# Optimization experiments

Hardware: AMD Instinct MI355X
Metric: run time of the kernel (lower is better)

Reference implementation:

```python
import jax, jax.numpy as jnp
import numpy as np

N, E = 50000, 800000
IN, C, H, EDIM = 128, 16, 8, 8  # in_channels, out_channels per head, heads, edge_dim
NEG_SLOPE = 0.2


def setup_inputs() -> dict:
    key = jax.random.key(0)
    ks = jax.random.split(key, 10)
    g = 1.0 / np.sqrt(IN)
    inp = {
        "x": jax.random.normal(ks[0], (N, IN), dtype=jnp.float32),
        "edge_index": jax.random.randint(ks[1], (2, E), 0, N, dtype=jnp.int64),
        "edge_attr": jax.random.normal(ks[2], (E, EDIM), dtype=jnp.float32),
        # GATv2Conv params (share_weights=False): lin_l, lin_r with bias, lin_edge no bias
        "W_l": jax.random.normal(ks[3], (IN, H * C), dtype=jnp.float32) * g,
        "b_l": jnp.zeros((H * C,), dtype=jnp.float32),
        "W_r": jax.random.normal(ks[4], (IN, H * C), dtype=jnp.float32) * g,
        "b_r": jnp.zeros((H * C,), dtype=jnp.float32),
        "W_e": jax.random.normal(ks[5], (EDIM, H * C), dtype=jnp.float32) * (1.0 / np.sqrt(EDIM)),
        "att": jax.random.normal(ks[6], (H, C), dtype=jnp.float32) * (1.0 / np.sqrt(C)),
        "bias": jnp.zeros((H * C,), dtype=jnp.float32),
    }
    return inp


def _gatv2_forward(x, edge_index, edge_attr, W_l, b_l, W_r, b_r, W_e, att, bias):
    n = x.shape[0]
    x_l = (x @ W_l + b_l).reshape(n, H, C)  # source transform
    x_r = (x @ W_r + b_r).reshape(n, H, C)  # target transform

    # add self-loops; edge_attr fill_value='mean' (PyG GATv2Conv default)
    loop = jnp.arange(n, dtype=edge_index.dtype)
    src = jnp.concatenate([edge_index[0], loop])
    dst = jnp.concatenate([edge_index[1], loop])
    loop_attr = jnp.broadcast_to(edge_attr.mean(axis=0, keepdims=True), (n, EDIM))
    e_attr = jnp.concatenate([edge_attr, loop_attr], axis=0)  # [E+N, EDIM]

    e_emb = (e_attr @ W_e).reshape(-1, H, C)  # [E+N, H, C]
    m = x_l[src] + x_r[dst] + e_emb          # gather per edge
    m = jax.nn.leaky_relu(m, NEG_SLOPE)
    logit = jnp.einsum("ehc,hc->eh", m, att)  # [E+N, H]

    # destination-grouped (scatter) softmax
    seg_max = jax.ops.segment_max(logit, dst, num_segments=n)
    expd = jnp.exp(logit - seg_max[dst])
    seg_sum = jax.ops.segment_sum(expd, dst, num_segments=n)
    alpha = expd / (seg_sum[dst] + 1e-16)     # [E+N, H]

    msg = alpha[:, :, None] * x_l[src]        # [E+N, H, C]
    out = jax.ops.segment_sum(msg, dst, num_segments=n)  # [N, H, C]
    return out.reshape(n, H * C) + bias       # concat heads + bias


def reference(x, edge_index, edge_attr, W_l, b_l, W_r, b_r, W_e, att, bias):
    return _gatv2_forward(x, edge_index, edge_attr, W_l, b_l, W_r, b_r, W_e, att, bias)
```

## Files before the change

kernel.cpp:

```cpp
#include <hip/hip_runtime.h>

#define NHEAD 8
#define CH    16
#define HC    128
#define INC   128
#define EDIM  8
#define NEG   0.2f

typedef _Float16 h8 __attribute__((ext_vector_type(8)));
typedef _Float16 h4 __attribute__((ext_vector_type(4)));
typedef _Float16 h2 __attribute__((ext_vector_type(2)));
typedef float    f4 __attribute__((ext_vector_type(4)));

__device__ __forceinline__ float lrelu(float v) { return v > 0.f ? v : NEG * v; }

__device__ __forceinline__ float dot2(h2 a, h2 b, float c) {
#if __has_builtin(__builtin_amdgcn_fdot2)
    return __builtin_amdgcn_fdot2(a, b, c, false);
#else
    return c + (float)a[0] * (float)b[0] + (float)a[1] * (float)b[1];
#endif
}

__global__ void k_packW(const float* __restrict__ Wl, const float* __restrict__ Wr,
                        _Float16* __restrict__ packed) {
    int id = blockIdx.x * blockDim.x + threadIdx.x;
    int l  = id & 63;
    int kb = (id >> 6) & 3;
    int t  = id >> 8;
    int col = t * 16 + (l & 15);
    const float* W = (col < HC) ? Wl : Wr;
    int c = col & 127;
    int kbase = kb * 32 + (l >> 4) * 8;
    _Float16* dst = packed + (size_t)id * 8;
    #pragma unroll
    for (int j = 0; j < 8; ++j) dst[j] = (_Float16)W[(size_t)(kbase + j) * HC + c];
}

__global__ __launch_bounds__(256) void k_phase1(
        const float* __restrict__ x, const _Float16* __restrict__ packed,
        const float* __restrict__ bl, const float* __restrict__ br,
        _Float16* __restrict__ xh,
        const int* __restrict__ ei, const float* __restrict__ ea,
        int* __restrict__ cnt, int* __restrict__ rank, float* __restrict__ attr_sum,
        int N, int E, int gemmBlocks) {
    __shared__ _Float16 st[16][264];
    __shared__ float red[4][8];

    if ((int)blockIdx.x < gemmBlocks) {
        int nb0 = blockIdx.x * 128;
        int w  = threadIdx.x >> 6;
        int l  = threadIdx.x & 63;

        const h8* pk = (const h8*)packed;
        h8 bfrag[4][4];
        #pragma unroll
        for (int t4 = 0; t4 < 4; ++t4)
            #pragma unroll
            for (int kb = 0; kb < 4; ++kb)
                bfrag[t4][kb] = pk[(size_t)(((w * 4 + t4) * 4 + kb) * 64 + l)];

        float bv[4];
        int cl = l & 15;
        #pragma unroll
        for (int t4 = 0; t4 < 4; ++t4) {
            int col = w * 64 + t4 * 16 + cl;
            bv[t4] = (col < HC) ? bl[col] : br[col - HC];
        }

        int g = l >> 4;
        int r0 = g * 4;
        for (int mt = 0; mt < 8; ++mt) {
            int m0 = nb0 + mt * 16;
            if (m0 >= N) break;
            int row = m0 + cl; if (row >= N) row = N - 1;
            const float* xp = x + (size_t)row * INC + g * 8;
            h8 afrag[4];
            #pragma unroll
            for (int kb = 0; kb < 4; ++kb) {
                float4 u = *(const float4*)(xp + kb * 32);
                float4 v = *(const float4*)(xp + kb * 32 + 4);
                h8 a;
                a[0] = (_Float16)u.x; a[1] = (_Float16)u.y; a[2] = (_Float16)u.z; a[3] = (_Float16)u.w;
                a[4] = (_Float16)v.x; a[5] = (_Float16)v.y; a[6] = (_Float16)v.z; a[7] = (_Float16)v.w;
                afrag[kb] = a;
            }
            f4 acc[4];
            #pragma unroll
            for (int t4 = 0; t4 < 4; ++t4) { f4 z = {0.f, 0.f, 0.f, 0.f}; acc[t4] = z; }
            #pragma unroll
            for (int kb = 0; kb < 4; ++kb)
                #pragma unroll
                for (int t4 = 0; t4 < 4; ++t4)
                    acc[t4] = __builtin_amdgcn_mfma_f32_16x16x32_f16(afrag[kb], bfrag[t4][kb], acc[t4], 0, 0, 0);
            #pragma unroll
            for (int t4 = 0; t4 < 4; ++t4) {
                int col = w * 64 + t4 * 16 + cl;
                #pragma unroll
                for (int j = 0; j < 4; ++j)
                    st[r0 + j][col] = (_Float16)(acc[t4][j] + bv[t4]);
            }
            __syncthreads();
            #pragma unroll
            for (int q = 0; q < 2; ++q) {
                int cch = threadIdx.x + 256 * q;
                int r = cch >> 5, ch = (cch & 31) * 8;
                int node = m0 + r;
                if (node < N) *(h8*)(xh + (size_t)node * 256 + ch) = *(const h8*)&st[r][ch];
            }
            __syncthreads();
        }
    } else {
        int t = (blockIdx.x - gemmBlocks) * 256 + threadIdx.x;
        float av[8] = {0.f, 0.f, 0.f, 0.f, 0.f, 0.f, 0.f, 0.f};
        if (t < E) {
            rank[t] = atomicAdd(&cnt[ei[E + t]], 1);
            float4 a0 = *(const float4*)(ea + (size_t)t * EDIM);
            float4 a1 = *(const float4*)(ea + (size_t)t * EDIM + 4);
            av[0] = a0.x; av[1] = a0.y; av[2] = a0.z; av[3] = a0.w;
            av[4] = a1.x; av[5] = a1.y; av[6] = a1.z; av[7] = a1.w;
        }
        #pragma unroll
        for (int m = 1; m < 64; m <<= 1) {
            #pragma unroll
            for (int k = 0; k < 8; ++k) av[k] += __shfl_xor(av[k], m);
        }
        int lane = threadIdx.x & 63, wid = threadIdx.x >> 6;
        if (lane == 0) {
            #pragma unroll
            for (int k = 0; k < 8; ++k) red[wid][k] = av[k];
        }
        __syncthreads();
        if (threadIdx.x < 8) {
            float s = red[0][threadIdx.x] + red[1][threadIdx.x] + red[2][threadIdx.x] + red[3][threadIdx.x];
            atomicAdd(&attr_sum[threadIdx.x], s);
        }
    }
}

__global__ void k_scan1(const int* __restrict__ cnt, int* __restrict__ off,
                        int* __restrict__ bsum, int N) {
    __shared__ int wpre[16];
    int i = blockIdx.x * 1024 + threadIdx.x;
    int lane = threadIdx.x & 63, wid = threadIdx.x >> 6;
    int v = (i < N) ? cnt[i] : 0;
    int s = v;
    #pragma unroll
    for (int d = 1; d < 64; d <<= 1) {
        int t = __shfl_up(s, d);
        if (lane >= d) s += t;
    }
    if (lane == 63) wpre[wid] = s;
    __syncthreads();
    if (threadIdx.x == 0) {
        int run = 0;
        #pragma unroll
        for (int q = 0; q < 16; ++q) { int t = wpre[q]; wpre[q] = run; run += t; }
        bsum[blockIdx.x] = run;
    }
    __syncthreads();
    if (i <= N) off[i] = wpre[wid] + s - v;
}

__global__ void k_scan2lo(const int* __restrict__ bsum, int* __restrict__ bsx, int nb,
                          const float* __restrict__ attr_sum, const float* __restrict__ We,
                          const float* __restrict__ att, float* __restrict__ loop_emb,
                          _Float16* __restrict__ We16, _Float16* __restrict__ att16,
                          float invE) {
    int tid = threadIdx.x;
    if (tid < 64) {
        int v = (tid < nb) ? bsum[tid] : 0;
        int s = v;
        #pragma unroll
        for (int d = 1; d < 64; d <<= 1) {
            int t = __shfl_up(s, d);
            if (tid >= d) s += t;
        }
        if (tid < nb) bsx[tid] = s - v;
    } else if (tid < 192) {
        int j = tid - 64;
        float acc = 0.f;
        #pragma unroll
        for (int d = 0; d < EDIM; ++d) {
            float w = We[d * HC + j];
            acc += attr_sum[d] * invE * w;
            We16[d * HC + j] = (_Float16)w;
        }
        loop_emb[j] = acc;
        att16[j] = (_Float16)att[j];
    }
}

__global__ void k_scatter(const int* __restrict__ ei, const float* __restrict__ ea,
                          const int* __restrict__ off, const int* __restrict__ bsx,
                          const int* __restrict__ rank,
                          int* __restrict__ esrc, h8* __restrict__ eac, int E) {
    int t = blockIdx.x * blockDim.x + threadIdx.x;
    if (t >= E) return;
    int dst = ei[E + t];
    int pos = off[dst] + bsx[dst >> 10] + rank[t];
    esrc[pos] = ei[t];
    float4 a0 = *(const float4*)(ea + (size_t)t * EDIM);
    float4 a1 = *(const float4*)(ea + (size_t)t * EDIM + 4);
    h8 v;
    v[0] = (_Float16)a0.x; v[1] = (_Float16)a0.y; v[2] = (_Float16)a0.z; v[3] = (_Float16)a0.w;
    v[4] = (_Float16)a1.x; v[5] = (_Float16)a1.y; v[6] = (_Float16)a1.z; v[7] = (_Float16)a1.w;
    eac[pos] = v;
}

__global__ __launch_bounds__(256) void k_gather(
        const int* __restrict__ esrc, const h8* __restrict__ eac,
        const _Float16* __restrict__ We16, const _Float16* __restrict__ att16,
        const float* __restrict__ attf, const _Float16* __restrict__ xh,
        const float* __restrict__ loop_emb, const float* __restrict__ bias,
        const int* __restrict__ off, const int* __restrict__ bsx,
        float* __restrict__ out, int N) {
    int wave = (blockIdx.x * blockDim.x + threadIdx.x) >> 6;
    int lane = threadIdx.x & 63;
    if (wave >= N) return;
    int dst = __builtin_amdgcn_readfirstlane(wave);
    int qid = lane >> 4;
    int l   = lane & 15;
    int c0  = l * 8;

    h8 we8[EDIM];
    #pragma unroll
    for (int d = 0; d < EDIM; ++d) we8[d] = *(const h8*)(We16 + d * HC + c0);
    h2 att2[4];
    #pragma unroll
    for (int k = 0; k < 4; ++k) att2[k] = *(const h2*)(att16 + c0 + 2 * k);
    h8 xr8 = *(const h8*)(xh + (size_t)dst * 256 + HC + c0);

    const h8 z8 = {};
    h8 ng8;
    #pragma unroll
    for (int k = 0; k < 8; ++k) ng8[k] = (_Float16)NEG;

    float accv[8] = {0.f, 0.f, 0.f, 0.f, 0.f, 0.f, 0.f, 0.f};
    float segw = 0.f;

    auto PROC = [&](h8 a8, h8 x8, bool cond) {
        h8 e8 = {};
        #pragma unroll
        for (int d = 0; d < EDIM; ++d) {
            h8 ad = {a8[d], a8[d], a8[d], a8[d], a8[d], a8[d], a8[d], a8[d]};
            e8 += ad * we8[d];
        }
        h8 m8 = x8 + xr8 + e8;
        h8 mp = __builtin_elementwise_max(m8, z8);
        h8 mn = __builtin_elementwise_min(m8, z8);
        m8 = mp + mn * ng8;
        float p = 0.f;
        #pragma unroll
        for (int k = 0; k < 4; ++k) {
            h2 mm; mm[0] = m8[2 * k]; mm[1] = m8[2 * k + 1];
            p = dot2(mm, att2[k], p);
        }
        p += __shfl_xor(p, 1);
        float w = cond ? __expf(p) : 0.f;
        segw += w;
        #pragma unroll
        for (int k = 0; k < 8; ++k) accv[k] += w * (float)x8[k];
    };

    {
        h8 xl8 = *(const h8*)(xh + (size_t)dst * 256 + c0);
        f4 le0 = *(const f4*)(loop_emb + c0), le1 = *(const f4*)(loop_emb + c0 + 4);
        f4 af0 = *(const f4*)(attf + c0),     af1 = *(const f4*)(attf + c0 + 4);
        float le[8] = {le0[0], le0[1], le0[2], le0[3], le1[0], le1[1], le1[2], le1[3]};
        float af[8] = {af0[0], af0[1], af0[2], af0[3], af1[0], af1[1], af1[2], af1[3]};
        float xf[8];
        float p = 0.f;
        #pragma unroll
        for (int k = 0; k < 8; ++k) {
            xf[k] = (float)xl8[k];
            p += lrelu(xf[k] + (float)xr8[k] + le[k]) * af[k];
        }
        p += __shfl_xor(p, 1);
        float w = (qid == 0) ? __expf(p) : 0.f;
        segw += w;
        #pragma unroll
        for (int k = 0; k < 8; ++k) accv[k] += w * xf[k];
    }

    int beg = off[dst] + bsx[dst >> 10];
    int end = off[dst + 1] + bsx[(dst + 1) >> 10];
    if (beg < end) {
        int last = end - 1;
        int j;
        j = beg + qid;          if (j > last) j = last;
        int sU = esrc[j]; h8 aU = eac[j];
        j = beg + 4 + qid;      if (j > last) j = last;
        int sV = esrc[j]; h8 aV = eac[j];
        h8 xU = *(const h8*)(xh + (size_t)sU * 256 + c0);
        h8 xV = *(const h8*)(xh + (size_t)sV * 256 + c0);
        j = beg + 8 + qid;      if (j > last) j = last;
        int sP = esrc[j];
        j = beg + 12 + qid;     if (j > last) j = last;
        int sQ = esrc[j];
        for (int i = beg; i < end; i += 8) {
            PROC(aU, xU, (i + qid) < end);
            {
                int jx = i + 8 + qid;  if (jx > last) jx = last;
                xU = *(const h8*)(xh + (size_t)sP * 256 + c0);
                aU = eac[jx];
                int jf = i + 16 + qid; if (jf > last) jf = last;
                sP = esrc[jf];
            }
            PROC(aV, xV, (i + 4 + qid) < end);
            {
                int jx = i + 12 + qid; if (jx > last) jx = last;
                xV = *(const h8*)(xh + (size_t)sQ * 256 + c0);
                aV = eac[jx];
                int jf = i + 20 + qid; if (jf > last) jf = last;
                sQ = esrc[jf];
            }
        }
    }

    segw += __shfl_xor(segw, 16); segw += __shfl_xor(segw, 32);
    #pragma unroll
    for (int k = 0; k < 8; ++k) {
        accv[k] += __shfl_xor(accv[k], 16);
        accv[k] += __shfl_xor(accv[k], 32);
    }

    if (qid == 0) {
        float inv = 1.f / (segw + 1e-16f);
        f4 b0 = *(const f4*)(bias + c0), b1 = *(const f4*)(bias + c0 + 4);
        f4 o0, o1;
        o0[0] = accv[0] * inv + b0[0]; o0[1] = accv[1] * inv + b0[1];
        o0[2] = accv[2] * inv + b0[2]; o0[3] = accv[3] * inv + b0[3];
        o1[0] = accv[4] * inv + b1[0]; o1[1] = accv[5] * inv + b1[1];
        o1[2] = accv[6] * inv + b1[2]; o1[3] = accv[7] * inv + b1[3];
        *(f4*)(out + (size_t)dst * HC + c0)     = o0;
        *(f4*)(out + (size_t)dst * HC + c0 + 4) = o1;
    }
}

extern "C" void kernel_launch(void* const* d_in, const int* in_sizes, int n_in,
                              void* d_out, int out_size, void* d_ws, size_t ws_size,
                              hipStream_t stream) {
    int N = in_sizes[0] / INC;
    int E = in_sizes[1] / 2;
    const float* x    = (const float*)d_in[0];
    const int*   ei   = (const int*)d_in[1];
    const float* ea   = (const float*)d_in[2];
    const float* Wl   = (const float*)d_in[3];
    const float* bl   = (const float*)d_in[4];
    const float* Wr   = (const float*)d_in[5];
    const float* br   = (const float*)d_in[6];
    const float* We   = (const float*)d_in[7];
    const float* att  = (const float*)d_in[8];
    const float* bias = (const float*)d_in[9];
    float* out = (float*)d_out;

    _Float16* xh      = (_Float16*)d_ws;
    h8*       eac     = (h8*)(xh + (size_t)N * 256);
    float* attr_sum   = (float*)(eac + E);
    int*   cnt        = (int*)(attr_sum + 8);
    float* loop_emb   = (float*)(cnt + N);
    _Float16* packed  = (_Float16*)(loop_emb + HC);
    _Float16* We16    = packed + 32768;
    _Float16* att16   = We16 + 1024;
    int*   off        = (int*)(att16 + 128);
    int*   rank       = off + (N + 2);
    int*   esrc       = rank + E;
    int*   bsum       = esrc + E;
    int*   bsx        = bsum + 64;

    hipMemsetAsync(attr_sum, 0, (8 + (size_t)N) * sizeof(float), stream);

    k_packW<<<16, 256, 0, stream>>>(Wl, Wr, packed);

    int gemmBlocks = (N + 127) / 128;
    int histBlocks = (E + 255) / 256;
    k_phase1<<<gemmBlocks + histBlocks, 256, 0, stream>>>(x, packed, bl, br, xh,
                                                          ei, ea, cnt, rank, attr_sum,
                                                          N, E, gemmBlocks);

    int nb = (N + 1 + 1023) / 1024;
    k_scan1<<<nb, 1024, 0, stream>>>(cnt, off, bsum, N);
    k_scan2lo<<<1, 256, 0, stream>>>(bsum, bsx, nb, attr_sum, We, att,
                                     loop_emb, We16, att16, 1.0f / (float)E);
    k_scatter<<<histBlocks, 256, 0, stream>>>(ei, ea, off, bsx, rank, esrc, eac, E);

    k_gather<<<(N * 64 + 255) / 256, 256, 0, stream>>>(esrc, eac, We16, att16, att, xh,
                                                       loop_emb, bias, off, bsx, out, N);
}
```

Measured before the change: 167.4 us.

## Fold block-sum scan into consumers, drop scan kernel, two destinations per wave

Removes the separate single-block scan kernel. Each wave in the scatter and gather kernels now recomputes the block-offset prefix from bsum with a wave-level scan, and the We/att fp16 conversion moves into the pack kernel. The loop embedding is stored in fp16 and computed in scan1. The gather kernel now handles two destination nodes per wave with a simpler one-ahead prefetch instead of the previous double-buffered prefetch, and the GEMM tiles drop to 64 rows per block. This saves one launch and one dependency step, but adds redundant scan work per wave, makes the loop-edge logit fp16, and reduces memory-latency hiding in gather.

```diff
diff --git a/kernel.cpp b/kernel.cpp
--- a/kernel.cpp
+++ b/kernel.cpp
@@ -8,11 +8,8 @@
 #define NEG   0.2f
 
 typedef _Float16 h8 __attribute__((ext_vector_type(8)));
-typedef _Float16 h4 __attribute__((ext_vector_type(4)));
 typedef _Float16 h2 __attribute__((ext_vector_type(2)));
 typedef float    f4 __attribute__((ext_vector_type(4)));
-
-__device__ __forceinline__ float lrelu(float v) { return v > 0.f ? v : NEG * v; }
 
 __device__ __forceinline__ float dot2(h2 a, h2 b, float c) {
 #if __has_builtin(__builtin_amdgcn_fdot2)
@@ -23,7 +20,9 @@
 }
 
 __global__ void k_packW(const float* __restrict__ Wl, const float* __restrict__ Wr,
-                        _Float16* __restrict__ packed) {
+                        const float* __restrict__ We, const float* __restrict__ att,
+                        _Float16* __restrict__ packed,
+                        _Float16* __restrict__ We16, _Float16* __restrict__ att16) {
     int id = blockIdx.x * blockDim.x + threadIdx.x;
     int l  = id & 63;
     int kb = (id >> 6) & 3;
@@ -35,6 +34,8 @@
     _Float16* dst = packed + (size_t)id * 8;
     #pragma unroll
     for (int j = 0; j < 8; ++j) dst[j] = (_Float16)W[(size_t)(kbase + j) * HC + c];
+    if (id < 1024) We16[id] = (_Float16)We[id];
+    if (id < 128)  att16[id] = (_Float16)att[id];
 }
 
 __global__ __launch_bounds__(256) void k_phase1(
@@ -48,7 +49,7 @@
     __shared__ float red[4][8];
 
     if ((int)blockIdx.x < gemmBlocks) {
-        int nb0 = blockIdx.x * 128;
+        int nb0 = blockIdx.x * 64;
         int w  = threadIdx.x >> 6;
         int l  = threadIdx.x & 63;
 
@@ -70,7 +71,7 @@
 
         int g = l >> 4;
         int r0 = g * 4;
-        for (int mt = 0; mt < 8; ++mt) {
+        for (int mt = 0; mt < 4; ++mt) {
             int m0 = nb0 + mt * 16;
             if (m0 >= N) break;
             int row = m0 + cl; if (row >= N) row = N - 1;
@@ -139,7 +140,9 @@
 }
 
 __global__ void k_scan1(const int* __restrict__ cnt, int* __restrict__ off,
-                        int* __restrict__ bsum, int N) {
+                        int* __restrict__ bsum, int N,
+                        const float* __restrict__ attr_sum, const float* __restrict__ We,
+                        _Float16* __restrict__ loop16, float invE) {
     __shared__ int wpre[16];
     int i = blockIdx.x * 1024 + threadIdx.x;
     int lane = threadIdx.x & 63, wid = threadIdx.x >> 6;
@@ -160,45 +163,34 @@
     }
     __syncthreads();
     if (i <= N) off[i] = wpre[wid] + s - v;
-}
-
-__global__ void k_scan2lo(const int* __restrict__ bsum, int* __restrict__ bsx, int nb,
-                          const float* __restrict__ attr_sum, const float* __restrict__ We,
-                          const float* __restrict__ att, float* __restrict__ loop_emb,
-                          _Float16* __restrict__ We16, _Float16* __restrict__ att16,
-                          float invE) {
-    int tid = threadIdx.x;
-    if (tid < 64) {
-        int v = (tid < nb) ? bsum[tid] : 0;
-        int s = v;
-        #pragma unroll
-        for (int d = 1; d < 64; d <<= 1) {
-            int t = __shfl_up(s, d);
-            if (tid >= d) s += t;
-        }
-        if (tid < nb) bsx[tid] = s - v;
-    } else if (tid < 192) {
-        int j = tid - 64;
+
+    if (blockIdx.x == 0 && threadIdx.x < HC) {
+        int j = threadIdx.x;
         float acc = 0.f;
         #pragma unroll
-        for (int d = 0; d < EDIM; ++d) {
-            float w = We[d * HC + j];
-            acc += attr_sum[d] * invE * w;
-            We16[d * HC + j] = (_Float16)w;
-        }
-        loop_emb[j] = acc;
-        att16[j] = (_Float16)att[j];
+        for (int d = 0; d < EDIM; ++d) acc += attr_sum[d] * invE * We[d * HC + j];
+        loop16[j] = (_Float16)acc;
     }
 }
 
 __global__ void k_scatter(const int* __restrict__ ei, const float* __restrict__ ea,
-                          const int* __restrict__ off, const int* __restrict__ bsx,
+                          const int* __restrict__ off, const int* __restrict__ bsum,
                           const int* __restrict__ rank,
-                          int* __restrict__ esrc, h8* __restrict__ eac, int E) {
+                          int* __restrict__ esrc, h8* __restrict__ eac, int E, int nb) {
+    int lane = threadIdx.x & 63;
+    int bv = (lane < nb) ? bsum[lane] : 0;
+    int s = bv;
+    #pragma unroll
+    for (int d = 1; d < 64; d <<= 1) {
+        int t = __shfl_up(s, d);
+        if (lane >= d) s += t;
+    }
+    s -= bv;
+
     int t = blockIdx.x * blockDim.x + threadIdx.x;
     if (t >= E) return;
     int dst = ei[E + t];
-    int pos = off[dst] + bsx[dst >> 10] + rank[t];
+    int pos = off[dst] + __shfl(s, dst >> 10) + rank[t];
     esrc[pos] = ei[t];
     float4 a0 = *(const float4*)(ea + (size_t)t * EDIM);
     float4 a1 = *(const float4*)(ea + (size_t)t * EDIM + 4);
@@ -211,130 +203,115 @@
 __global__ __launch_bounds__(256) void k_gather(
         const int* __restrict__ esrc, const h8* __restrict__ eac,
         const _Float16* __restrict__ We16, const _Float16* __restrict__ att16,
-        const float* __restrict__ attf, const _Float16* __restrict__ xh,
-        const float* __restrict__ loop_emb, const float* __restrict__ bias,
-        const int* __restrict__ off, const int* __restrict__ bsx,
-        float* __restrict__ out, int N) {
-    int wave = (blockIdx.x * blockDim.x + threadIdx.x) >> 6;
+        const _Float16* __restrict__ xh, const _Float16* __restrict__ loop16,
+        const float* __restrict__ bias,
+        const int* __restrict__ off, const int* __restrict__ bsum,
+        float* __restrict__ out, int N, int nb) {
+    int wid = (blockIdx.x * blockDim.x + threadIdx.x) >> 6;
     int lane = threadIdx.x & 63;
-    if (wave >= N) return;
-    int dst = __builtin_amdgcn_readfirstlane(wave);
+    int dst0 = wid * 2;
+    if (dst0 >= N) return;
     int qid = lane >> 4;
     int l   = lane & 15;
     int c0  = l * 8;
 
+    int bv = (lane < nb) ? bsum[lane] : 0;
+    int sx = bv;
+    #pragma unroll
+    for (int d = 1; d < 64; d <<= 1) {
+        int t = __shfl_up(sx, d);
+        if (lane >= d) sx += t;
+    }
+    sx -= bv;
+
     h8 we8[EDIM];
     #pragma unroll
     for (int d = 0; d < EDIM; ++d) we8[d] = *(const h8*)(We16 + d * HC + c0);
+    h8 av8 = *(const h8*)(att16 + c0);
     h2 att2[4];
     #pragma unroll
-    for (int k = 0; k < 4; ++k) att2[k] = *(const h2*)(att16 + c0 + 2 * k);
-    h8 xr8 = *(const h8*)(xh + (size_t)dst * 256 + HC + c0);
-
+    for (int k = 0; k < 4; ++k) { att2[k][0] = av8[2 * k]; att2[k][1] = av8[2 * k + 1]; }
+    h8 lp8 = *(const h8*)(loop16 + c0);
     const h8 z8 = {};
     h8 ng8;
     #pragma unroll
     for (int k = 0; k < 8; ++k) ng8[k] = (_Float16)NEG;
 
-    float accv[8] = {0.f, 0.f, 0.f, 0.f, 0.f, 0.f, 0.f, 0.f};
-    float segw = 0.f;
-
-    auto PROC = [&](h8 a8, h8 x8, bool cond) {
-        h8 e8 = {};
-        #pragma unroll
-        for (int d = 0; d < EDIM; ++d) {
-            h8 ad = {a8[d], a8[d], a8[d], a8[d], a8[d], a8[d], a8[d], a8[d]};
-            e8 += ad * we8[d];
-        }
-        h8 m8 = x8 + xr8 + e8;
-        h8 mp = __builtin_elementwise_max(m8, z8);
-        h8 mn = __builtin_elementwise_min(m8, z8);
-        m8 = mp + mn * ng8;
-        float p = 0.f;
-        #pragma unroll
-        for (int k = 0; k < 4; ++k) {
-            h2 mm; mm[0] = m8[2 * k]; mm[1] = m8[2 * k + 1];
-            p = dot2(mm, att2[k], p);
-        }
-        p += __shfl_xor(p, 1);
-        float w = cond ? __expf(p) : 0.f;
-        segw += w;
-        #pragma unroll
-        for (int k = 0; k < 8; ++k) accv[k] += w * (float)x8[k];
-    };
-
-    {
-        h8 xl8 = *(const h8*)(xh + (size_t)dst * 256 + c0);
-        f4 le0 = *(const f4*)(loop_emb + c0), le1 = *(const f4*)(loop_emb + c0 + 4);
-        f4 af0 = *(const f4*)(attf + c0),     af1 = *(const f4*)(attf + c0 + 4);
-        float le[8] = {le0[0], le0[1], le0[2], le0[3], le1[0], le1[1], le1[2], le1[3]};
-        float af[8] = {af0[0], af0[1], af0[2], af0[3], af1[0], af1[1], af1[2], af1[3]};
-        float xf[8];
-        float p = 0.f;
+    for (int rep = 0; rep < 2; ++rep) {
+        int dst = dst0 + rep;
+        if (dst >= N) break;
+        dst = __builtin_amdgcn_readfirstlane(dst);
+
+        h8 xr8 = *(const h8*)(xh + (size_t)dst * 256 + HC + c0);
+
+        float accv[8] = {0.f, 0.f, 0.f, 0.f, 0.f, 0.f, 0.f, 0.f};
+        float segw = 0.f;
+
+        auto TAIL = [&](h8 m8, h8 x8, bool valid) {
+            h8 mp = __builtin_elementwise_max(m8, z8);
+            h8 mn = __builtin_elementwise_min(m8, z8);
+            m8 = mp + mn * ng8;
+            float p = 0.f;
+            #pragma unroll
+            for (int k = 0; k < 4; ++k) {
+                h2 mm; mm[0] = m8[2 * k]; mm[1] = m8[2 * k + 1];
+                p = dot2(mm, att2[k], p);
+            }
+            p += __shfl_xor(p, 1);
+            float w = valid ? __expf(p) : 0.f;
+            segw += w;
+            #pragma unroll
+            for (int k = 0; k < 8; ++k) accv[k] += w * (float)x8[k];
+        };
+
+        {
+            h8 x8 = *(const h8*)(xh + (size_t)dst * 256 + c0);
+            TAIL(x8 + xr8 + lp8, x8, qid == 0);
+        }
+
+        int q0 = dst >> 10, q1 = (dst + 1) >> 10;
+        int beg = off[dst] + __shfl(sx, q0);
+        int end = off[dst + 1] + __shfl(sx, q1);
+        if (beg < end) {
+            int last = end - 1;
+            int j = beg + qid; if (j > last) j = last;
+            int s0 = esrc[j];
+            h8 a0 = eac[j];
+            h8 x0 = *(const h8*)(xh + (size_t)s0 * 256 + c0);
+            for (int i = beg; i < end; i += 4) {
+                int jn = i + 4 + qid; if (jn > last) jn = last;
+                int sn = esrc[jn];
+                h8 an = eac[jn];
+                h8 xn = *(const h8*)(xh + (size_t)sn * 256 + c0);
+                h8 m8 = x0 + xr8;
+                #pragma unroll
+                for (int d = 0; d < EDIM; ++d) {
+                    h8 ad = {a0[d], a0[d], a0[d], a0[d], a0[d], a0[d], a0[d], a0[d]};
+                    m8 += ad * we8[d];
+                }
+                TAIL(m8, x0, (i + qid) < end);
+                a0 = an; x0 = xn;
+            }
+        }
+
+        segw += __shfl_xor(segw, 16); segw += __shfl_xor(segw, 32);
         #pragma unroll
         for (int k = 0; k < 8; ++k) {
-            xf[k] = (float)xl8[k];
-            p += lrelu(xf[k] + (float)xr8[k] + le[k]) * af[k];
-        }
-        p += __shfl_xor(p, 1);
-        float w = (qid == 0) ? __expf(p) : 0.f;
-        segw += w;
-        #pragma unroll
-        for (int k = 0; k < 8; ++k) accv[k] += w * xf[k];
-    }
-
-    int beg = off[dst] + bsx[dst >> 10];
-    int end = off[dst + 1] + bsx[(dst + 1) >> 10];
-    if (beg < end) {
-        int last = end - 1;
-        int j;
-        j = beg + qid;          if (j > last) j = last;
-        int sU = esrc[j]; h8 aU = eac[j];
-        j = beg + 4 + qid;      if (j > last) j = last;
-        int sV = esrc[j]; h8 aV = eac[j];
-        h8 xU = *(const h8*)(xh + (size_t)sU * 256 + c0);
-        h8 xV = *(const h8*)(xh + (size_t)sV * 256 + c0);
-        j = beg + 8 + qid;      if (j > last) j = last;
-        int sP = esrc[j];
-        j = beg + 12 + qid;     if (j > last) j = last;
-        int sQ = esrc[j];
-        for (int i = beg; i < end; i += 8) {
-            PROC(aU, xU, (i + qid) < end);
-            {
-                int jx = i + 8 + qid;  if (jx > last) jx = last;
-                xU = *(const h8*)(xh + (size_t)sP * 256 + c0);
-                aU = eac[jx];
-                int jf = i + 16 + qid; if (jf > last) jf = last;
-                sP = esrc[jf];
-            }
-            PROC(aV, xV, (i + 4 + qid) < end);
-            {
-                int jx = i + 12 + qid; if (jx > last) jx = last;
-                xV = *(const h8*)(xh + (size_t)sQ * 256 + c0);
-                aV = eac[jx];
-                int jf = i + 20 + qid; if (jf > last) jf = last;
-                sQ = esrc[jf];
-            }
-        }
-    }
-
-    segw += __shfl_xor(segw, 16); segw += __shfl_xor(segw, 32);
-    #pragma unroll
-    for (int k = 0; k < 8; ++k) {
-        accv[k] += __shfl_xor(accv[k], 16);
-        accv[k] += __shfl_xor(accv[k], 32);
-    }
-
-    if (qid == 0) {
-        float inv = 1.f / (segw + 1e-16f);
-        f4 b0 = *(const f4*)(bias + c0), b1 = *(const f4*)(bias + c0 + 4);
-        f4 o0, o1;
-        o0[0] = accv[0] * inv + b0[0]; o0[1] = accv[1] * inv + b0[1];
-        o0[2] = accv[2] * inv + b0[2]; o0[3] = accv[3] * inv + b0[3];
-        o1[0] = accv[4] * inv + b1[0]; o1[1] = accv[5] * inv + b1[1];
-        o1[2] = accv[6] * inv + b1[2]; o1[3] = accv[7] * inv + b1[3];
-        *(f4*)(out + (size_t)dst * HC + c0)     = o0;
-        *(f4*)(out + (size_t)dst * HC + c0 + 4) = o1;
+            accv[k] += __shfl_xor(accv[k], 16);
+            accv[k] += __shfl_xor(accv[k], 32);
+        }
+
+        if (qid == 0) {
+            float inv = 1.f / (segw + 1e-16f);
+            f4 b0 = *(const f4*)(bias + c0), b1 = *(const f4*)(bias + c0 + 4);
+            f4 o0, o1;
+            o0[0] = accv[0] * inv + b0[0]; o0[1] = accv[1] * inv + b0[1];
+            o0[2] = accv[2] * inv + b0[2]; o0[3] = accv[3] * inv + b0[3];
+            o1[0] = accv[4] * inv + b1[0]; o1[1] = accv[5] * inv + b1[1];
+            o1[2] = accv[6] * inv + b1[2]; o1[3] = accv[7] * inv + b1[3];
+            *(f4*)(out + (size_t)dst * HC + c0)     = o0;
+            *(f4*)(out + (size_t)dst * HC + c0 + 4) = o1;
+        }
     }
 }
 
@@ -359,32 +336,31 @@
     h8*       eac     = (h8*)(xh + (size_t)N * 256);
     float* attr_sum   = (float*)(eac + E);
     int*   cnt        = (int*)(attr_sum + 8);
-    float* loop_emb   = (float*)(cnt + N);
-    _Float16* packed  = (_Float16*)(loop_emb + HC);
+    _Float16* loop16  = (_Float16*)(cnt + N);
+    _Float16* packed  = loop16 + 128;
     _Float16* We16    = packed + 32768;
     _Float16* att16   = We16 + 1024;
     int*   off        = (int*)(att16 + 128);
     int*   rank       = off + (N + 2);
     int*   esrc       = rank + E;
     int*   bsum       = esrc + E;
-    int*   bsx        = bsum + 64;
 
     hipMemsetAsync(attr_sum, 0, (8 + (size_t)N) * sizeof(float), stream);
 
-    k_packW<<<16, 256, 0, stream>>>(Wl, Wr, packed);
-
-    int gemmBlocks = (N + 127) / 128;
+    k_packW<<<16, 256, 0, stream>>>(Wl, Wr, We, att, packed, We16, att16);
+
+    int gemmBlocks = (N + 63) / 64;
     int histBlocks = (E + 255) / 256;
     k_phase1<<<gemmBlocks + histBlocks, 256, 0, stream>>>(x, packed, bl, br, xh,
                                                           ei, ea, cnt, rank, attr_sum,
                                                           N, E, gemmBlocks);
 
     int nb = (N + 1 + 1023) / 1024;
-    k_scan1<<<nb, 1024, 0, stream>>>(cnt, off, bsum, N);
-    k_scan2lo<<<1, 256, 0, stream>>>(bsum, bsx, nb, attr_sum, We, att,
-                                     loop_emb, We16, att16, 1.0f / (float)E);
-    k_scatter<<<histBlocks, 256, 0, stream>>>(ei, ea, off, bsx, rank, esrc, eac, E);
-
-    k_gather<<<(N * 64 + 255) / 256, 256, 0, stream>>>(esrc, eac, We16, att16, att, xh,
-                                                       loop_emb, bias, off, bsx, out, N);
-}
+    k_scan1<<<nb, 1024, 0, stream>>>(cnt, off, bsum, N, attr_sum, We, loop16, 1.0f / (float)E);
+
+    k_scatter<<<histBlocks, 256, 0, stream>>>(ei, ea, off, bsum, rank, esrc, eac, E, nb);
+
+    int waves = (N + 1) / 2;
+    k_gather<<<(waves * 64 + 255) / 256, 256, 0, stream>>>(esrc, eac, We16, att16, xh, loop16,
+                                                           bias, off, bsum, out, N, nb);
+}
```

Measured after the change: 168.0 us. No clear change (+0.3%).
